# Optimization experiments

Measured on AMD Instinct MI355X. Metric: run time of the kernel, lower is better.

Reference implementation:

```python
import jax, jax.numpy as jnp
import numpy as np

N = 5
B = 1048576
RANGE = jnp.asarray([np.pi / 2, np.pi, np.pi / 2, np.pi, np.pi / 2], dtype=jnp.float32)
NUM_STEPS = 10


def setup_inputs() -> dict:
    key = jax.random.key(0)
    ks = jax.random.split(key, 9)
    return {
        "obs": jax.random.normal(ks[0], (B, 10), dtype=jnp.float32),
        "t": jax.random.uniform(ks[1], (B,), dtype=jnp.float32) * 10.0,
        "dt": jnp.full((1,), 0.01, dtype=jnp.float32),
        "mu_p": jax.random.normal(ks[2], (N,), dtype=jnp.float32),
        "a": jax.random.normal(ks[3], (N,), dtype=jnp.float32),
        "w": jax.random.normal(ks[4], (N, N), dtype=jnp.float32),
        "phi": jax.random.normal(ks[5], (N, N), dtype=jnp.float32),
        "frequencies": jax.random.normal(ks[6], (N,), dtype=jnp.float32),
        "amplitudes": jax.random.normal(ks[7], (N,), dtype=jnp.float32),
        "phases": jax.random.normal(ks[8], (N,), dtype=jnp.float32),
        "std": jnp.ones((N,), dtype=jnp.float32) * 0.5,
    }


def _dynamics(r, r_dot, theta, mu_p, a, w, phi, frequencies):
    # r, r_dot, theta: [b, N]
    r_dot_dot = a * (a / 4 * (mu_p - r) - r_dot)
    # diff[b,i,j] = theta_j - theta_i - phi_ij
    diff = theta[:, None, :] - theta[:, :, None] - phi[None, :, :]
    coupling = jnp.einsum("ij,bij,bj->bi", w, jnp.sin(diff), r)
    theta_dot = frequencies[None, :] + coupling
    return r_dot_dot, theta_dot


def _rk4_step(r, r_dot, theta, dt, mu_p, a, w, phi, frequencies):
    rdd1, td1 = _dynamics(r, r_dot, theta, mu_p, a, w, phi, frequencies)
    k1_r, k1_rd, k1_t = r_dot, rdd1, td1
    rdd2, td2 = _dynamics(r + 0.5 * dt * k1_r, r_dot + 0.5 * dt * k1_rd, theta + 0.5 * dt * k1_t,
                          mu_p, a, w, phi, frequencies)
    k2_r, k2_rd, k2_t = r_dot + 0.5 * dt * k1_rd, rdd2, td2
    rdd3, td3 = _dynamics(r + 0.5 * dt * k2_r, r_dot + 0.5 * dt * k2_rd, theta + 0.5 * dt * k2_t,
                          mu_p, a, w, phi, frequencies)
    k3_r, k3_rd, k3_t = r_dot + 0.5 * dt * k2_rd, rdd3, td3
    rdd4, td4 = _dynamics(r + dt * k3_r, r_dot + dt * k3_rd, theta + dt * k3_t,
                          mu_p, a, w, phi, frequencies)
    k4_r, k4_rd, k4_t = r_dot + dt * k3_rd, rdd4, td4
    r = r + dt / 6 * (k1_r + 2 * k2_r + 2 * k3_r + k4_r)
    r_dot = r_dot + dt / 6 * (k1_rd + 2 * k2_rd + 2 * k3_rd + k4_rd)
    theta = theta + dt / 6 * (k1_t + 2 * k2_t + 2 * k3_t + k4_t)
    return r, r_dot, theta


def reference(obs, t, dt, mu_p, a, w, phi, frequencies, amplitudes, phases, std):
    b = t.shape[0]
    dt_s = dt[0]
    r = jnp.zeros((b, N), dtype=t.dtype)
    r_dot = jnp.zeros_like(r)
    theta = jnp.zeros_like(r)

    def body(_, carry):
        r, r_dot, theta = carry
        return _rk4_step(r, r_dot, theta, dt_s, mu_p, a, w, phi, frequencies)

    r, r_dot, theta = jax.lax.fori_loop(0, NUM_STEPS, body, (r, r_dot, theta))

    f = jax.nn.softplus(frequencies)                 # true frequencies
    amp = jnp.tanh(amplitudes) * RANGE               # true amplitudes
    p = jax.nn.softplus(phases)                      # true phases
    two_pi = jnp.float32(2.0 * np.pi)
    mu = amp[None, :] * jnp.sin(two_pi * f[None, :] * t[:, None] + p[None, :])  # [b, N]
    std_full = jnp.ones_like(mu) * std[None, :]
    # stack distribution params + live CPG state: [4, b, N]
    return jnp.stack([mu, std_full, r, theta], axis=0)
```

## Files before the change

### kernel.cpp

```cpp
#include <hip/hip_runtime.h>
#include <math.h>

constexpr int kN      = 5;
constexpr int kB      = 1048576;
constexpr int kBN     = kB * kN;
constexpr int kBN4    = kBN / 4;
constexpr int kSteps  = 10;
constexpr int kBlocks = 1280;
constexpr int kThreads = 256;

__device__ __forceinline__ void cpg_dynamics(float r, float rd, float th,
                                             float mu, float a,
                                             const float wr[kN], const float ph[kN],
                                             float freq, float& rdd, float& thd)
{
    rdd = a * (a * 0.25f * (mu - r) - rd);
    float coup = 0.f;
#pragma unroll
    for (int j = 0; j < kN; ++j) {
        float th_j = __shfl(th, j);
        float r_j  = __shfl(r, j);
        coup = __builtin_fmaf(wr[j] * __sinf(th_j - th - ph[j]), r_j, coup);
    }
    thd = freq + coup;
}

__device__ __forceinline__ float softplus_f(float x)
{
    return fmaxf(x, 0.f) + log1pf(expf(-fabsf(x)));
}

__global__ __launch_bounds__(kThreads)
void ijspeert_kernel(const float* __restrict__ t,
                     const float* __restrict__ dt_p,
                     const float* __restrict__ mu_p,
                     const float* __restrict__ a_p,
                     const float* __restrict__ w_p,
                     const float* __restrict__ phi_p,
                     const float* __restrict__ freq_p,
                     const float* __restrict__ amp_p,
                     const float* __restrict__ phase_p,
                     const float* __restrict__ std_p,
                     float* __restrict__ out)
{
    __shared__ float s_amp[kN], s_w2[kN], s_p[kN], s_std[kN], s_r[kN], s_th[kN];

    if (threadIdx.x < 64) {
        const int i = (threadIdx.x < kN) ? (int)threadIdx.x : 0;
        const float dt = dt_p[0];
        const float mu = mu_p[i];
        const float a  = a_p[i];
        const float fr = freq_p[i];
        float wr[kN], ph[kN];
#pragma unroll
        for (int j = 0; j < kN; ++j) {
            wr[j] = w_p[i * kN + j];
            ph[j] = phi_p[i * kN + j];
        }

        float r = 0.f, rd = 0.f, th = 0.f;
        for (int s = 0; s < kSteps; ++s) {
            float rdd1, td1, rdd2, td2, rdd3, td3, rdd4, td4;
            cpg_dynamics(r, rd, th, mu, a, wr, ph, fr, rdd1, td1);
            const float k1_r = rd, k1_rd = rdd1, k1_t = td1;
            cpg_dynamics(r + 0.5f * dt * k1_r, rd + 0.5f * dt * k1_rd,
                         th + 0.5f * dt * k1_t, mu, a, wr, ph, fr, rdd2, td2);
            const float k2_r = rd + 0.5f * dt * k1_rd, k2_rd = rdd2, k2_t = td2;
            cpg_dynamics(r + 0.5f * dt * k2_r, rd + 0.5f * dt * k2_rd,
                         th + 0.5f * dt * k2_t, mu, a, wr, ph, fr, rdd3, td3);
            const float k3_r = rd + 0.5f * dt * k2_rd, k3_rd = rdd3, k3_t = td3;
            cpg_dynamics(r + dt * k3_r, rd + dt * k3_rd,
                         th + dt * k3_t, mu, a, wr, ph, fr, rdd4, td4);
            const float k4_r = rd + dt * k3_rd, k4_rd = rdd4, k4_t = td4;
            const float c = dt * (1.f / 6.f);
            r  += c * (k1_r  + 2.f * k2_r  + 2.f * k3_r  + k4_r);
            rd += c * (k1_rd + 2.f * k2_rd + 2.f * k3_rd + k4_rd);
            th += c * (k1_t  + 2.f * k2_t  + 2.f * k3_t  + k4_t);
        }

        if (threadIdx.x < kN) {
            const float pi  = 3.14159265358979323846f;
            const float rng = (i & 1) ? pi : (0.5f * pi);
            const float f_true = softplus_f(fr);
            s_w2[i]  = 2.f * pi * f_true;
            s_amp[i] = tanhf(amp_p[i]) * rng;
            s_p[i]   = softplus_f(phase_p[i]);
            s_std[i] = std_p[i];
            s_r[i]   = r;
            s_th[i]  = th;
        }
    }
    __syncthreads();

    const unsigned stride = kBlocks * kThreads;
    unsigned gid = blockIdx.x * kThreads + threadIdx.x;
    float4* o = reinterpret_cast<float4*>(out);

    for (unsigned q = gid; q < (unsigned)kBN4; q += stride) {
        const unsigned f0 = q * 4u;
        float vm[4], vs[4], vr[4], vt[4];
#pragma unroll
        for (int k = 0; k < 4; ++k) {
            const unsigned fk = f0 + (unsigned)k;
            const unsigned b  = fk / 5u;
            const unsigned i  = fk - b * 5u;
            const float tb  = t[b];
            const float arg = __builtin_fmaf(s_w2[i], tb, s_p[i]);
            vm[k] = s_amp[i] * __sinf(arg);
            vs[k] = s_std[i];
            vr[k] = s_r[i];
            vt[k] = s_th[i];
        }
        o[q]                = make_float4(vm[0], vm[1], vm[2], vm[3]);
        o[kBN4 + q]         = make_float4(vs[0], vs[1], vs[2], vs[3]);
        o[2 * kBN4 + q]     = make_float4(vr[0], vr[1], vr[2], vr[3]);
        o[3 * kBN4 + q]     = make_float4(vt[0], vt[1], vt[2], vt[3]);
    }
}

extern "C" void kernel_launch(void* const* d_in, const int* in_sizes, int n_in,
                              void* d_out, int out_size, void* d_ws, size_t ws_size,
                              hipStream_t stream)
{
    const float* t      = (const float*)d_in[1];
    const float* dt     = (const float*)d_in[2];
    const float* mu_p   = (const float*)d_in[3];
    const float* a      = (const float*)d_in[4];
    const float* w      = (const float*)d_in[5];
    const float* phi    = (const float*)d_in[6];
    const float* freq   = (const float*)d_in[7];
    const float* amp    = (const float*)d_in[8];
    const float* phase  = (const float*)d_in[9];
    const float* stdv   = (const float*)d_in[10];
    float* out = (float*)d_out;

    ijspeert_kernel<<<kBlocks, kThreads, 0, stream>>>(
        t, dt, mu_p, a, w, phi, freq, amp, phase, stdv, out);
}
```

Measured before the change: 140.6 us.

## Assign four batch rows per thread and overlap RK4 with mu/std stores

Replaces the grid-stride loop with one thread per four batch rows (20 outputs), which removes the per-element division by 5 and the shared-memory lookups. Every wavefront now runs the tiny 5-oscillator RK4 integration redundantly, after issuing its mu and std stores, so the serial integration no longer sits in front of the memory traffic and the __syncthreads goes away. Each thread reads t as a single float4 and writes five contiguous float4s per output plane. The cost is 10 RK4 steps per wavefront instead of one per block, plus more registers per thread, and the stores within a wave are now strided by 80 bytes per lane rather than fully contiguous.

```diff
diff --git a/kernel.cpp b/kernel.cpp
--- a/kernel.cpp
+++ b/kernel.cpp
@@ -6,8 +6,13 @@
 constexpr int kBN     = kB * kN;
 constexpr int kBN4    = kBN / 4;
 constexpr int kSteps  = 10;
-constexpr int kBlocks = 1280;
 constexpr int kThreads = 256;
+constexpr int kBlocks  = kB / (4 * kThreads);
+
+__device__ __forceinline__ float softplus_f(float x)
+{
+    return fmaxf(x, 0.f) + log1pf(expf(-fabsf(x)));
+}
 
 __device__ __forceinline__ void cpg_dynamics(float r, float rd, float th,
                                              float mu, float a,
@@ -25,11 +30,6 @@
     thd = freq + coup;
 }
 
-__device__ __forceinline__ float softplus_f(float x)
-{
-    return fmaxf(x, 0.f) + log1pf(expf(-fabsf(x)));
-}
-
 __global__ __launch_bounds__(kThreads)
 void ijspeert_kernel(const float* __restrict__ t,
                      const float* __restrict__ dt_p,
@@ -43,79 +43,94 @@
                      const float* __restrict__ std_p,
                      float* __restrict__ out)
 {
-    __shared__ float s_amp[kN], s_w2[kN], s_p[kN], s_std[kN], s_r[kN], s_th[kN];
+    const int tid  = blockIdx.x * kThreads + (int)threadIdx.x;
+    const int lane = (int)(threadIdx.x & 63u);
+    const int i    = (lane < kN) ? lane : 0;
 
-    if (threadIdx.x < 64) {
-        const int i = (threadIdx.x < kN) ? (int)threadIdx.x : 0;
-        const float dt = dt_p[0];
-        const float mu = mu_p[i];
-        const float a  = a_p[i];
-        const float fr = freq_p[i];
-        float wr[kN], ph[kN];
+    const float pi = 3.14159265358979323846f;
+    const float fr = freq_p[i];
+    const float my_w2  = 2.f * pi * softplus_f(fr);
+    const float my_amp = tanhf(amp_p[i]) * ((i & 1) ? pi : 0.5f * pi);
+    const float my_ph  = softplus_f(phase_p[i]);
+    const float my_sd  = std_p[i];
+
+    float amp[kN], w2[kN], pp[kN], sd[kN];
 #pragma unroll
-        for (int j = 0; j < kN; ++j) {
-            wr[j] = w_p[i * kN + j];
-            ph[j] = phi_p[i * kN + j];
-        }
+    for (int j = 0; j < kN; ++j) {
+        amp[j] = __shfl(my_amp, j);
+        w2[j]  = __shfl(my_w2,  j);
+        pp[j]  = __shfl(my_ph,  j);
+        sd[j]  = __shfl(my_sd,  j);
+    }
 
-        float r = 0.f, rd = 0.f, th = 0.f;
-        for (int s = 0; s < kSteps; ++s) {
-            float rdd1, td1, rdd2, td2, rdd3, td3, rdd4, td4;
-            cpg_dynamics(r, rd, th, mu, a, wr, ph, fr, rdd1, td1);
-            const float k1_r = rd, k1_rd = rdd1, k1_t = td1;
-            cpg_dynamics(r + 0.5f * dt * k1_r, rd + 0.5f * dt * k1_rd,
-                         th + 0.5f * dt * k1_t, mu, a, wr, ph, fr, rdd2, td2);
-            const float k2_r = rd + 0.5f * dt * k1_rd, k2_rd = rdd2, k2_t = td2;
-            cpg_dynamics(r + 0.5f * dt * k2_r, rd + 0.5f * dt * k2_rd,
-                         th + 0.5f * dt * k2_t, mu, a, wr, ph, fr, rdd3, td3);
-            const float k3_r = rd + 0.5f * dt * k2_rd, k3_rd = rdd3, k3_t = td3;
-            cpg_dynamics(r + dt * k3_r, rd + dt * k3_rd,
-                         th + dt * k3_t, mu, a, wr, ph, fr, rdd4, td4);
-            const float k4_r = rd + dt * k3_rd, k4_rd = rdd4, k4_t = td4;
-            const float c = dt * (1.f / 6.f);
-            r  += c * (k1_r  + 2.f * k2_r  + 2.f * k3_r  + k4_r);
-            rd += c * (k1_rd + 2.f * k2_rd + 2.f * k3_rd + k4_rd);
-            th += c * (k1_t  + 2.f * k2_t  + 2.f * k3_t  + k4_t);
-        }
+    float4* o = reinterpret_cast<float4*>(out);
+    const int q0 = tid * 5;
 
-        if (threadIdx.x < kN) {
-            const float pi  = 3.14159265358979323846f;
-            const float rng = (i & 1) ? pi : (0.5f * pi);
-            const float f_true = softplus_f(fr);
-            s_w2[i]  = 2.f * pi * f_true;
-            s_amp[i] = tanhf(amp_p[i]) * rng;
-            s_p[i]   = softplus_f(phase_p[i]);
-            s_std[i] = std_p[i];
-            s_r[i]   = r;
-            s_th[i]  = th;
-        }
+    {
+        const float4 tv = reinterpret_cast<const float4*>(t)[tid];
+        const float tb[4] = {tv.x, tv.y, tv.z, tv.w};
+
+        float4 m4[5];
+        float* m = reinterpret_cast<float*>(m4);
+#pragma unroll
+        for (int bb = 0; bb < 4; ++bb)
+#pragma unroll
+            for (int j = 0; j < kN; ++j)
+                m[bb * 5 + j] = amp[j] * __sinf(__builtin_fmaf(w2[j], tb[bb], pp[j]));
+#pragma unroll
+        for (int k = 0; k < 5; ++k) o[q0 + k] = m4[k];
+
+        float4 s4[5];
+        float* s = reinterpret_cast<float*>(s4);
+#pragma unroll
+        for (int k = 0; k < 20; ++k) s[k] = sd[k % 5];
+#pragma unroll
+        for (int k = 0; k < 5; ++k) o[kBN4 + q0 + k] = s4[k];
     }
-    __syncthreads();
 
-    const unsigned stride = kBlocks * kThreads;
-    unsigned gid = blockIdx.x * kThreads + threadIdx.x;
-    float4* o = reinterpret_cast<float4*>(out);
+    float wr[kN], ph[kN];
+#pragma unroll
+    for (int j = 0; j < kN; ++j) {
+        wr[j] = w_p[i * kN + j];
+        ph[j] = phi_p[i * kN + j];
+    }
+    const float dt = dt_p[0];
+    const float mu = mu_p[i];
+    const float a  = a_p[i];
 
-    for (unsigned q = gid; q < (unsigned)kBN4; q += stride) {
-        const unsigned f0 = q * 4u;
-        float vm[4], vs[4], vr[4], vt[4];
+    float r = 0.f, rd = 0.f, th = 0.f;
+    for (int s = 0; s < kSteps; ++s) {
+        float rdd1, td1, rdd2, td2, rdd3, td3, rdd4, td4;
+        cpg_dynamics(r, rd, th, mu, a, wr, ph, fr, rdd1, td1);
+        const float k1_r = rd, k1_rd = rdd1, k1_t = td1;
+        cpg_dynamics(r + 0.5f * dt * k1_r, rd + 0.5f * dt * k1_rd,
+                     th + 0.5f * dt * k1_t, mu, a, wr, ph, fr, rdd2, td2);
+        const float k2_r = rd + 0.5f * dt * k1_rd, k2_rd = rdd2, k2_t = td2;
+        cpg_dynamics(r + 0.5f * dt * k2_r, rd + 0.5f * dt * k2_rd,
+                     th + 0.5f * dt * k2_t, mu, a, wr, ph, fr, rdd3, td3);
+        const float k3_r = rd + 0.5f * dt * k2_rd, k3_rd = rdd3, k3_t = td3;
+        cpg_dynamics(r + dt * k3_r, rd + dt * k3_rd,
+                     th + dt * k3_t, mu, a, wr, ph, fr, rdd4, td4);
+        const float k4_r = rd + dt * k3_rd, k4_rd = rdd4, k4_t = td4;
+        const float c = dt * (1.f / 6.f);
+        r  += c * (k1_r  + 2.f * k2_r  + 2.f * k3_r  + k4_r);
+        rd += c * (k1_rd + 2.f * k2_rd + 2.f * k3_rd + k4_rd);
+        th += c * (k1_t  + 2.f * k2_t  + 2.f * k3_t  + k4_t);
+    }
+
+    float rr[kN], tt[kN];
 #pragma unroll
-        for (int k = 0; k < 4; ++k) {
-            const unsigned fk = f0 + (unsigned)k;
-            const unsigned b  = fk / 5u;
-            const unsigned i  = fk - b * 5u;
-            const float tb  = t[b];
-            const float arg = __builtin_fmaf(s_w2[i], tb, s_p[i]);
-            vm[k] = s_amp[i] * __sinf(arg);
-            vs[k] = s_std[i];
-            vr[k] = s_r[i];
-            vt[k] = s_th[i];
-        }
-        o[q]                = make_float4(vm[0], vm[1], vm[2], vm[3]);
-        o[kBN4 + q]         = make_float4(vs[0], vs[1], vs[2], vs[3]);
-        o[2 * kBN4 + q]     = make_float4(vr[0], vr[1], vr[2], vr[3]);
-        o[3 * kBN4 + q]     = make_float4(vt[0], vt[1], vt[2], vt[3]);
-    }
+    for (int j = 0; j < kN; ++j) { rr[j] = __shfl(r, j); tt[j] = __shfl(th, j); }
+
+    float4 r4[5], t4[5];
+    float* rp = reinterpret_cast<float*>(r4);
+    float* tp = reinterpret_cast<float*>(t4);
+#pragma unroll
+    for (int k = 0; k < 20; ++k) { rp[k] = rr[k % 5]; tp[k] = tt[k % 5]; }
+#pragma unroll
+    for (int k = 0; k < 5; ++k) o[2 * kBN4 + q0 + k] = r4[k];
+#pragma unroll
+    for (int k = 0; k < 5; ++k) o[3 * kBN4 + q0 + k] = t4[k];
 }
 
 extern "C" void kernel_launch(void* const* d_in, const int* in_sizes, int n_in,
```

Result: no change. 143.0 us (+1.7%).
